# Optimization experiments

Hardware: AMD Instinct MI355X
Metric: run time of the kernel (lower is better)

## Reference

```python
import jax, jax.numpy as jnp
import numpy as np

B, S = 4, 4096          # batch, tokens (64x64 SAM ViT-H grid)
DIN, DOUT = 1280, 3840  # qkv linear dims
RANK = 16
NUM_SHARED = 1
NUM_ROUTED = 6
TOP_K = 3


def setup_inputs() -> dict:
    key = jax.random.key(0)
    ks = jax.random.split(key, 9)
    s = 0.02
    return {
        "x": jax.random.normal(ks[0], (B, S, DIN), dtype=jnp.float32),
        "base_w": jax.random.normal(ks[1], (DIN, DOUT), dtype=jnp.float32) * s,
        "base_b": jax.random.normal(ks[2], (DOUT,), dtype=jnp.float32) * s,
        "shared_w1": jax.random.normal(ks[3], (NUM_SHARED, DIN, RANK), dtype=jnp.float32) * s,
        "shared_w2": jax.random.normal(ks[4], (NUM_SHARED, RANK, DOUT), dtype=jnp.float32) * s,
        "routed_w1": jax.random.normal(ks[5], (NUM_ROUTED, DIN, RANK), dtype=jnp.float32) * s,
        "routed_w2": jax.random.normal(ks[6], (NUM_ROUTED, RANK, DOUT), dtype=jnp.float32) * s,
        "router_w": jax.random.normal(ks[7], (DIN, NUM_ROUTED), dtype=jnp.float32) * s,
        "router_b": jax.random.normal(ks[8], (NUM_ROUTED,), dtype=jnp.float32) * s,
    }


def reference(x, base_w, base_b, shared_w1, shared_w2, routed_w1, routed_w2, router_w, router_b):
    b, s, din = x.shape
    # base linear runs under torch.no_grad() -> stop_gradient
    base = jax.lax.stop_gradient(jnp.einsum('bsi,io->bso', x, base_w) + base_b)
    # shared low-rank experts, summed over the shared set
    shared = jnp.einsum('bsi,eir,ero->bso', x, shared_w1, shared_w2)
    # router: softmax gates, top-k selection
    gates = jax.nn.softmax(x @ router_w + router_b, axis=-1)      # [B,S,E]
    topk_w, topk_idx = jax.lax.top_k(gates, TOP_K)                # [B,S,K]
    T = b * s
    xf = x.reshape(T, din)
    # combine weights: per-token weight for each expert (top-k indices are
    # distinct, so scatter-add reproduces the per-slot assignment exactly)
    cw = jnp.zeros((T, NUM_ROUTED), dtype=x.dtype).at[
        jnp.arange(T)[:, None], topk_idx.reshape(T, TOP_K)
    ].add(topk_w.reshape(T, TOP_K))                               # [T,E]
    # routed experts: contract rank and expert dims without materializing [T,E,DOUT]
    h = jnp.einsum('ti,eir->ter', xf, routed_w1)                  # [T,E,RANK]
    routed = jnp.einsum('ter,ero,te->to', h, routed_w2, cw).reshape(b, s, DOUT)
    return base + shared + routed
```

## Files before the change

### kernel.cpp

```cpp
#include <hip/hip_runtime.h>
#include <cstdint>
#include <cstddef>

#define DIN 1280
#define DOUT 3840
#define NEXP 6
#define RANK 16
#define TOKENS 16384
#define KPAD 1408
#define NLOW 128

typedef __bf16 bf16x8 __attribute__((ext_vector_type(8)));
typedef float f32x4 __attribute__((ext_vector_type(4)));
typedef unsigned short u16x8 __attribute__((ext_vector_type(8)));

#define SB() __builtin_amdgcn_sched_barrier(0)
#define BAR() __builtin_amdgcn_s_barrier()

__device__ __forceinline__ unsigned short f2bf(float f) {
    unsigned u = __builtin_bit_cast(unsigned, f);
    u += 0x7fff + ((u >> 16) & 1);
    return (unsigned short)(u >> 16);
}

__device__ __forceinline__ void async_load16(void* lds, const void* g) {
    __builtin_amdgcn_global_load_lds(
        (const __attribute__((address_space(1))) unsigned int*)g,
        (__attribute__((address_space(3))) unsigned int*)lds, 16, 0, 0);
}

__global__ void prep_w2t(const float* __restrict__ base_w,
                         const float* __restrict__ shared_w2,
                         const float* __restrict__ routed_w2,
                         unsigned short* __restrict__ WT) {
    __shared__ unsigned short tile[32][33];
    int k0 = blockIdx.x * 32, n0 = blockIdx.y * 32;
    int tx = threadIdx.x, ty = threadIdx.y;
#pragma unroll
    for (int j = 0; j < 4; j++) {
        int k = k0 + ty + j * 8;
        int n = n0 + tx;
        float v;
        if (k < DIN)            v = base_w[(size_t)k * DOUT + n];
        else if (k < DIN + 16)  v = shared_w2[(size_t)(k - DIN) * DOUT + n];
        else if (k < DIN + 112) v = routed_w2[(size_t)(k - DIN - 16) * DOUT + n];
        else                    v = 0.f;
        tile[ty + j * 8][tx] = f2bf(v);
    }
    __syncthreads();
#pragma unroll
    for (int j = 0; j < 4; j++) {
        int n = n0 + ty + j * 8;
        int k = k0 + tx;
        WT[(size_t)n * KPAD + k] = tile[tx][ty + j * 8];
    }
}

__global__ void prep_w1t(const float* __restrict__ shared_w1,
                         const float* __restrict__ routed_w1,
                         unsigned short* __restrict__ W1T) {
    __shared__ unsigned short tile[32][33];
    int k0 = blockIdx.x * 32, n0 = blockIdx.y * 32;
    int tx = threadIdx.x, ty = threadIdx.y;
#pragma unroll
    for (int j = 0; j < 4; j++) {
        int k = k0 + ty + j * 8;
        int n = n0 + tx;
        float v = 0.f;
        if (n < 16) v = shared_w1[k * RANK + n];
        else if (n < 112) {
            int jj = n - 16, e = jj >> 4, r = jj & 15;
            v = routed_w1[(size_t)e * DIN * RANK + k * RANK + r];
        }
        tile[ty + j * 8][tx] = f2bf(v);
    }
    __syncthreads();
#pragma unroll
    for (int j = 0; j < 4; j++) {
        int n = n0 + ty + j * 8;
        int k = k0 + tx;
        W1T[(size_t)n * DIN + k] = tile[tx][ty + j * 8];
    }
}

__global__ __launch_bounds__(256) void router_kernel(
    const float* __restrict__ x,
    const float* __restrict__ router_w,
    const float* __restrict__ router_b,
    unsigned short* __restrict__ A,
    float* __restrict__ cw) {
    int tid = threadIdx.x;
    size_t t0 = (size_t)blockIdx.x * 8;
    const float* xblk = x + t0 * DIN;
    unsigned short* Ablk = A + t0 * KPAD;

    for (int i = tid; i < 8 * (DIN / 8); i += 256) {
        int t = i / (DIN / 8), c = (i - t * (DIN / 8)) * 8;
        const float* xs = xblk + (size_t)t * DIN + c;
        f32x4 v0 = *(const f32x4*)xs;
        f32x4 v1 = *(const f32x4*)(xs + 4);
        u16x8 o;
#pragma unroll
        for (int j = 0; j < 4; j++) { o[j] = f2bf(v0[j]); o[4 + j] = f2bf(v1[j]); }
        *(u16x8*)&Ablk[(size_t)t * KPAD + c] = o;
    }
    if (tid < 128) {
        int t = tid >> 4, c = tid & 15;
        Ablk[t * KPAD + DIN + 112 + c] = 0;
    }

    int tg = tid >> 5, lj = tid & 31;
    const float* xt = xblk + (size_t)tg * DIN;
    float acc[6] = {0.f, 0.f, 0.f, 0.f, 0.f, 0.f};
    for (int k = lj; k < DIN; k += 32) {
        float xv = xt[k];
        const float* wr = router_w + k * NEXP;
#pragma unroll
        for (int e = 0; e < NEXP; e++) acc[e] = fmaf(xv, wr[e], acc[e]);
    }
#pragma unroll
    for (int off = 16; off > 0; off >>= 1)
#pragma unroll
        for (int e = 0; e < NEXP; e++) acc[e] += __shfl_xor(acc[e], off);

    float mx = -1e30f;
#pragma unroll
    for (int e = 0; e < NEXP; e++) { acc[e] += router_b[e]; mx = fmaxf(mx, acc[e]); }
    float g[6]; float s = 0.f;
#pragma unroll
    for (int e = 0; e < NEXP; e++) { g[e] = __expf(acc[e] - mx); s += g[e]; }
    float inv = 1.f / s;
    if (lj < NEXP) {
        float ge = g[lj];
        int cnt = 0;
#pragma unroll
        for (int e = 0; e < NEXP; e++) {
            if (e == lj) continue;
            if (g[e] > ge || (g[e] == ge && e < lj)) cnt++;
        }
        cw[(t0 + tg) * NEXP + lj] = (cnt < 3) ? ge * inv : 0.f;
    }
}

__global__ __launch_bounds__(256) void combine_kernel(
    const float* __restrict__ H, const float* __restrict__ cw,
    unsigned short* __restrict__ A) {
    int i = blockIdx.x * 256 + threadIdx.x;
    int t = i / 112, j = i - t * 112;
    float h = H[(size_t)t * NLOW + j] + H[(size_t)TOKENS * NLOW + (size_t)t * NLOW + j];
    float f = (j < 16) ? 1.0f : cw[t * NEXP + ((j - 16) >> 4)];
    A[(size_t)t * KPAD + DIN + j] = f2bf(f * h);
}

__global__ __launch_bounds__(256, 2) void gemm_small(
    const unsigned short* __restrict__ A,
    const unsigned short* __restrict__ BT,
    float* __restrict__ H) {
    __shared__ unsigned short ldsA[128 * 32];
    __shared__ unsigned short ldsB[128 * 32];
    const int KS = DIN / 2;
    int tid = threadIdx.x;
    int lane = tid & 63, wave = tid >> 6;
    int m0 = blockIdx.y * 128;
    int z = blockIdx.z;
    int wm = (wave >> 1) * 64, wn = (wave & 1) * 64;
    int lr = lane & 15, quad = lane >> 4;

    f32x4 acc[4][4] = {};
    const unsigned short* Abase = A + (size_t)m0 * KPAD + z * KS;
    const unsigned short* Bbase = BT + z * KS;
    float* Cbase = H + (size_t)z * TOKENS * NLOW;

    for (int k0 = 0; k0 < KS; k0 += 32) {
#pragma unroll
        for (int i = 0; i < 2; i++) {
            int c = i * 256 + tid;
            int row = c >> 2;
            int col = (c & 3) << 3;
            async_load16(&ldsA[(i * 256 + wave * 64) * 8],
                         Abase + (size_t)row * KPAD + k0 + col);
            async_load16(&ldsB[(i * 256 + wave * 64) * 8],
                         Bbase + (size_t)row * DIN + k0 + col);
        }
        __syncthreads();
        bf16x8 af[4], bf[4];
#pragma unroll
        for (int mi = 0; mi < 4; mi++)
            af[mi] = *(const bf16x8*)&ldsA[(wm + mi * 16 + lr) * 32 + quad * 8];
#pragma unroll
        for (int ni = 0; ni < 4; ni++)
            bf[ni] = *(const bf16x8*)&ldsB[(wn + ni * 16 + lr) * 32 + quad * 8];
#pragma unroll
        for (int mi = 0; mi < 4; mi++)
#pragma unroll
            for (int ni = 0; ni < 4; ni++)
                acc[mi][ni] = __builtin_amdgcn_mfma_f32_16x16x32_bf16(
                    af[mi], bf[ni], acc[mi][ni], 0, 0, 0);
        __syncthreads();
    }
#pragma unroll
    for (int ni = 0; ni < 4; ni++) {
        int gn = wn + ni * 16 + lr;
#pragma unroll
        for (int mi = 0; mi < 4; mi++) {
            int gm = m0 + wm + mi * 16 + quad * 4;
            f32x4 v = acc[mi][ni];
#pragma unroll
            for (int r = 0; r < 4; r++)
                Cbase[(size_t)(gm + r) * NLOW + gn] = v[r];
        }
    }
}


#define READ_AQ(AQ, MB) do { \
    AQ[0][0] = rdA(a_cur, (MB) + 0, 0); AQ[0][1] = rdA(a_cur, (MB) + 0, 1); \
    AQ[1][0] = rdA(a_cur, (MB) + 1, 0); AQ[1][1] = rdA(a_cur, (MB) + 1, 1); \
} while (0)

#define MFMA_QUAD(AQ, MB) do { \
    _Pragma("unroll") for (int ks_ = 0; ks_ < 2; ks_++) \
    _Pragma("unroll") for (int mq_ = 0; mq_ < 2; mq_++) \
    _Pragma("unroll") for (int ni_ = 0; ni_ < 4; ni_++) \
        acc[(MB) + mq_][ni_] = __builtin_amdgcn_mfma_f32_16x16x32_bf16( \
            AQ[mq_][ks_], bfr[ni_][ks_], acc[(MB) + mq_][ni_], 0, 0, 0); \
} while (0)

__global__ __launch_bounds__(512, 2) void gemm256(
    const unsigned short* __restrict__ A,
    const unsigned short* __restrict__ BT,
    const float* __restrict__ bias,
    float* __restrict__ C) {
    __shared__ unsigned short lA[2][256 * 64];
    __shared__ unsigned short lB[2][256 * 64];

    int tid = threadIdx.x;
    int lane = tid & 63, wave = tid >> 6;
    int bid = blockIdx.x;
    int xcd = bid & 7, lid = bid >> 3;
    int mt = xcd * 8 + (lid & 7);
    int nt = lid >> 3;
    int m0 = mt * 256, n0 = nt * 256;

    int wm = (wave >> 2) * 128, wn = (wave & 3) * 64;
    int lr = lane & 15, quad = lane >> 4;
    int swz = (lr & 7) << 4;

    int sr = lane >> 3;
    int sc = (lane & 7) ^ sr;
    const unsigned short* aSrc = A + (size_t)(m0 + wave * 32 + sr) * KPAD + sc * 8;
    const unsigned short* bSrc = BT + (size_t)(n0 + wave * 32 + sr) * KPAD + sc * 8;

    auto stA2 = [&](unsigned short* dst, int k0, int pr) {
#pragma unroll
        for (int i = pr * 2; i < pr * 2 + 2; i++)
            async_load16(dst + (size_t)(wave * 32 + i * 8) * 64,
                         aSrc + (size_t)(i * 8) * KPAD + k0);
    };
    auto stB2 = [&](unsigned short* dst, int k0, int pr) {
#pragma unroll
        for (int i = pr * 2; i < pr * 2 + 2; i++)
            async_load16(dst + (size_t)(wave * 32 + i * 8) * 64,
                         bSrc + (size_t)(i * 8) * KPAD + k0);
    };
    auto rdA = [&](const unsigned short* base, int mi, int ks) -> bf16x8 {
        int row = wm + mi * 16 + lr;
        int off = row * 128 + (((ks << 6) | (quad << 4)) ^ swz);
        return *(const bf16x8*)((const char*)base + off);
    };
    auto rdB = [&](const unsigned short* base, int ni, int ks) -> bf16x8 {
        int row = wn + ni * 16 + lr;
        int off = row * 128 + (((ks << 6) | (quad << 4)) ^ swz);
        return *(const bf16x8*)((const char*)base + off);
    };

    f32x4 acc[8][4] = {};

    stA2(&lA[0][0], 0, 0);  stA2(&lA[0][0], 0, 1);
    stB2(&lB[0][0], 0, 0);  stB2(&lB[0][0], 0, 1);
    stA2(&lA[1][0], 64, 0); stA2(&lA[1][0], 64, 1);
    stB2(&lB[1][0], 64, 0); stB2(&lB[1][0], 64, 1);
    asm volatile("s_waitcnt vmcnt(8)" ::: "memory");
    SB(); BAR(); SB();

    const int nkt = KPAD / 64;
#pragma unroll 2
    for (int t = 0; t < nkt; ++t) {
        const int c = t & 1;
        unsigned short* a_cur = &lA[c][0];
        unsigned short* b_cur = &lB[c][0];
        int k0 = t * 64;
        const bool st_ok = (t + 2 < nkt);

        bf16x8 bfr[4][2];
        bf16x8 aq0[2][2], aq1[2][2], aq2[2][2], aq3[2][2];

#pragma unroll
        for (int ni = 0; ni < 4; ni++) {
            bfr[ni][0] = rdB(b_cur, ni, 0);
            bfr[ni][1] = rdB(b_cur, ni, 1);
        }
        SB();
        READ_AQ(aq0, 0);
        READ_AQ(aq1, 2);
        SB();
        asm volatile("s_waitcnt lgkmcnt(8)" ::: "memory");
        SB(); BAR(); SB();

        READ_AQ(aq2, 4);
        if (st_ok) stB2(b_cur, k0 + 128, 0);
        SB();
        __builtin_amdgcn_s_setprio(1); MFMA_QUAD(aq0, 0); __builtin_amdgcn_s_setprio(0);
        SB();

        READ_AQ(aq3, 6);
        if (st_ok) stB2(b_cur, k0 + 128, 1);
        SB();
        __builtin_amdgcn_s_setprio(1); MFMA_QUAD(aq1, 2); __builtin_amdgcn_s_setprio(0);
        SB();

        __builtin_amdgcn_s_setprio(1); MFMA_QUAD(aq2, 4); __builtin_amdgcn_s_setprio(0);
        SB();
        asm volatile("s_waitcnt lgkmcnt(0)" ::: "memory");
        SB(); BAR(); SB();

        if (st_ok) { stA2(a_cur, k0 + 128, 0); stA2(a_cur, k0 + 128, 1); }
        SB();
        __builtin_amdgcn_s_setprio(1); MFMA_QUAD(aq3, 6); __builtin_amdgcn_s_setprio(0);
        SB();
        if (st_ok) asm volatile("s_waitcnt vmcnt(8)" ::: "memory");
        else       asm volatile("s_waitcnt vmcnt(0)" ::: "memory");
        SB(); BAR(); SB();
    }

#pragma unroll
    for (int mi = 0; mi < 8; mi++) {
        int gm = m0 + wm + mi * 16 + quad * 4;
#pragma unroll
        for (int ni = 0; ni < 4; ni++) {
            int gn = n0 + wn + ni * 16 + lr;
            float bv = bias[gn];
            f32x4 v = acc[mi][ni];
#pragma unroll
            for (int r = 0; r < 4; r++)
                C[(size_t)(gm + r) * DOUT + gn] = v[r] + bv;
        }
    }
}

extern "C" void kernel_launch(void* const* d_in, const int* in_sizes, int n_in,
                              void* d_out, int out_size, void* d_ws, size_t ws_size,
                              hipStream_t stream) {
    const float* x         = (const float*)d_in[0];
    const float* base_w    = (const float*)d_in[1];
    const float* base_b    = (const float*)d_in[2];
    const float* shared_w1 = (const float*)d_in[3];
    const float* shared_w2 = (const float*)d_in[4];
    const float* routed_w1 = (const float*)d_in[5];
    const float* routed_w2 = (const float*)d_in[6];
    const float* router_w  = (const float*)d_in[7];
    const float* router_b  = (const float*)d_in[8];
    float* out = (float*)d_out;

    char* ws = (char*)d_ws;
    size_t off = 0;
    unsigned short* A     = (unsigned short*)(ws + off); off += (size_t)TOKENS * KPAD * 2;
    unsigned short* WcatT = (unsigned short*)(ws + off); off += (size_t)DOUT * KPAD * 2;
    unsigned short* W1T   = (unsigned short*)(ws + off); off += (size_t)NLOW * DIN * 2;
    float* H              = (float*)(ws + off);          off += (size_t)2 * TOKENS * NLOW * 4;
    float* cw             = (float*)(ws + off);          off += (size_t)TOKENS * NEXP * 4;

    prep_w2t<<<dim3(KPAD / 32, DOUT / 32), dim3(32, 8), 0, stream>>>(
        base_w, shared_w2, routed_w2, WcatT);
    prep_w1t<<<dim3(DIN / 32, NLOW / 32), dim3(32, 8), 0, stream>>>(
        shared_w1, routed_w1, W1T);
    router_kernel<<<TOKENS / 8, 256, 0, stream>>>(x, router_w, router_b, A, cw);
    gemm_small<<<dim3(1, TOKENS / 128, 2), 256, 0, stream>>>(A, W1T, H);
    combine_kernel<<<(TOKENS * 112) / 256, 256, 0, stream>>>(H, cw, A);
    gemm256<<<(TOKENS / 256) * (DOUT / 256), 512, 0, stream>>>(A, WcatT, base_b, out);
}
```

Before: 287.2 us.

## Interleave LDS fragment reads with MFMAs per k-half and cut one barrier

Restructures the GEMM inner loop so LDS fragments are read split by k-half, in small groups with fine-grained lgkmcnt waits between MFMA bursts. This lowers register pressure and overlaps LDS reads with matrix math. All four global-to-LDS stores for the next stage now happen after a single barrier, which removes one mid-iteration barrier. The cost is later store issue, since B stores no longer overlap the early MFMAs, and more waitcnt points that the scheduler must honour.

```diff
diff --git a/kernel.cpp b/kernel.cpp
--- a/kernel.cpp
+++ b/kernel.cpp
@@ -16,6 +16,7 @@
 
 #define SB() __builtin_amdgcn_sched_barrier(0)
 #define BAR() __builtin_amdgcn_s_barrier()
+#define LGKM(n) do { asm volatile("s_waitcnt lgkmcnt(" #n ")" ::: "memory"); SB(); } while (0)
 
 __device__ __forceinline__ unsigned short f2bf(float f) {
     unsigned u = __builtin_bit_cast(unsigned, f);
@@ -213,17 +214,13 @@
 }
 
 
-#define READ_AQ(AQ, MB) do { \
-    AQ[0][0] = rdA(a_cur, (MB) + 0, 0); AQ[0][1] = rdA(a_cur, (MB) + 0, 1); \
-    AQ[1][0] = rdA(a_cur, (MB) + 1, 0); AQ[1][1] = rdA(a_cur, (MB) + 1, 1); \
-} while (0)
-
-#define MFMA_QUAD(AQ, MB) do { \
-    _Pragma("unroll") for (int ks_ = 0; ks_ < 2; ks_++) \
+#define MFMA8(Q, MB, BF) do { \
+    __builtin_amdgcn_s_setprio(1); \
     _Pragma("unroll") for (int mq_ = 0; mq_ < 2; mq_++) \
     _Pragma("unroll") for (int ni_ = 0; ni_ < 4; ni_++) \
         acc[(MB) + mq_][ni_] = __builtin_amdgcn_mfma_f32_16x16x32_bf16( \
-            AQ[mq_][ks_], bfr[ni_][ks_], acc[(MB) + mq_][ni_], 0, 0, 0); \
+            Q[mq_], BF[ni_], acc[(MB) + mq_][ni_], 0, 0, 0); \
+    __builtin_amdgcn_s_setprio(0); SB(); \
 } while (0)
 
 __global__ __launch_bounds__(512, 2) void gemm256(
@@ -292,42 +289,59 @@
         int k0 = t * 64;
         const bool st_ok = (t + 2 < nkt);
 
-        bf16x8 bfr[4][2];
-        bf16x8 aq0[2][2], aq1[2][2], aq2[2][2], aq3[2][2];
-
-#pragma unroll
-        for (int ni = 0; ni < 4; ni++) {
-            bfr[ni][0] = rdB(b_cur, ni, 0);
-            bfr[ni][1] = rdB(b_cur, ni, 1);
-        }
-        SB();
-        READ_AQ(aq0, 0);
-        READ_AQ(aq1, 2);
-        SB();
-        asm volatile("s_waitcnt lgkmcnt(8)" ::: "memory");
+        bf16x8 b0[4], b1[4];
+        bf16x8 qA[2], qB[2], qC[2], qD[2];
+
+#pragma unroll
+        for (int ni = 0; ni < 4; ni++) b0[ni] = rdB(b_cur, ni, 0);
+        qA[0] = rdA(a_cur, 0, 0); qA[1] = rdA(a_cur, 1, 0);
+        qB[0] = rdA(a_cur, 2, 0); qB[1] = rdA(a_cur, 3, 0);
+        qC[0] = rdA(a_cur, 4, 0); qC[1] = rdA(a_cur, 5, 0);
+        SB();
+        LGKM(4);
+        MFMA8(qA, 0, b0);
+
+        qD[0] = rdA(a_cur, 6, 0); qD[1] = rdA(a_cur, 7, 0);
+        SB();
+        LGKM(4);
+        MFMA8(qB, 2, b0);
+
+#pragma unroll
+        for (int ni = 0; ni < 4; ni++) b1[ni] = rdB(b_cur, ni, 1);
+        SB();
+        LGKM(6);
+        MFMA8(qC, 4, b0);
+
+        qA[0] = rdA(a_cur, 0, 1); qA[1] = rdA(a_cur, 1, 1);
+        SB();
+        LGKM(6);
+        MFMA8(qD, 6, b0);
+
+        qB[0] = rdA(a_cur, 2, 1); qB[1] = rdA(a_cur, 3, 1);
+        SB();
+        LGKM(2);
+        MFMA8(qA, 0, b1);
+
+        qC[0] = rdA(a_cur, 4, 1); qC[1] = rdA(a_cur, 5, 1);
+        SB();
+        LGKM(2);
+        MFMA8(qB, 2, b1);
+
+        qD[0] = rdA(a_cur, 6, 1); qD[1] = rdA(a_cur, 7, 1);
+        SB();
+        LGKM(2);
+        MFMA8(qC, 4, b1);
+
+        LGKM(0);
         SB(); BAR(); SB();
 
-        READ_AQ(aq2, 4);
-        if (st_ok) stB2(b_cur, k0 + 128, 0);
-        SB();
-        __builtin_amdgcn_s_setprio(1); MFMA_QUAD(aq0, 0); __builtin_amdgcn_s_setprio(0);
-        SB();
-
-        READ_AQ(aq3, 6);
-        if (st_ok) stB2(b_cur, k0 + 128, 1);
-        SB();
-        __builtin_amdgcn_s_setprio(1); MFMA_QUAD(aq1, 2); __builtin_amdgcn_s_setprio(0);
-        SB();
-
-        __builtin_amdgcn_s_setprio(1); MFMA_QUAD(aq2, 4); __builtin_amdgcn_s_setprio(0);
-        SB();
-        asm volatile("s_waitcnt lgkmcnt(0)" ::: "memory");
-        SB(); BAR(); SB();
-
-        if (st_ok) { stA2(a_cur, k0 + 128, 0); stA2(a_cur, k0 + 128, 1); }
-        SB();
-        __builtin_amdgcn_s_setprio(1); MFMA_QUAD(aq3, 6); __builtin_amdgcn_s_setprio(0);
-        SB();
+        if (st_ok) {
+            stA2(a_cur, k0 + 128, 0); stA2(a_cur, k0 + 128, 1);
+            stB2(b_cur, k0 + 128, 0); stB2(b_cur, k0 + 128, 1);
+        }
+        SB();
+        MFMA8(qD, 6, b1);
+
         if (st_ok) asm volatile("s_waitcnt vmcnt(8)" ::: "memory");
         else       asm volatile("s_waitcnt vmcnt(0)" ::: "memory");
         SB(); BAR(); SB();
@@ -377,5 +391,6 @@
     router_kernel<<<TOKENS / 8, 256, 0, stream>>>(x, router_w, router_b, A, cw);
     gemm_small<<<dim3(1, TOKENS / 128, 2), 256, 0, stream>>>(A, W1T, H);
     combine_kernel<<<(TOKENS * 112) / 256, 256, 0, stream>>>(H, cw, A);
-    gemm256<<<(TOKENS / 256) * (DOUT / 256), 512, 0, stream>>>(A, WcatT, base_b, out);
-}
+    gemm256<<<(TOKENS / 256) * (DOUT / 256), 512, 0, stream>>>(
+        A, WcatT, base_b, out);
+}
```

Measured after the change: 300.2 us. 1.05x slower.
